# Kernel optimization log

Measured on AMD Instinct MI355X. Metric: run time of the kernel, lower is better.

Reference implementation:

```python
import jax, jax.numpy as jnp
import numpy as np

NUM_NODES = 100000
NUM_EDGES = 1600000
EMBED_DIM = 128
NUM_CLASSES = 2
NUM_LAYERS = 3


def setup_inputs() -> dict:
    key = jax.random.key(0)
    k_row, k_col, k_val, k_emb, k_a, k_w, k_b = jax.random.split(key, 7)
    node_indices = jnp.arange(NUM_NODES, dtype=jnp.int64 if jax.config.read('jax_enable_x64') else jnp.int32)
    adj_row = jax.random.randint(k_row, (NUM_EDGES,), 0, NUM_NODES)
    adj_col = jax.random.randint(k_col, (NUM_EDGES,), 0, NUM_NODES)
    # symmetric-normalized-ish positive edge weights
    adj_val = jax.random.uniform(k_val, (NUM_EDGES,), dtype=jnp.float32) * (1.0 / 16.0)
    embedding = jax.random.normal(k_emb, (NUM_NODES, EMBED_DIM), dtype=jnp.float32)
    alpha = jnp.ones((NUM_LAYERS + 1,), dtype=jnp.float32) / (NUM_LAYERS + 1)
    W = jax.random.normal(k_w, (EMBED_DIM, NUM_CLASSES), dtype=jnp.float32) * 0.05
    b = jnp.zeros((NUM_CLASSES,), dtype=jnp.float32)
    return {
        'node_indices': node_indices, 'adj_row': adj_row, 'adj_col': adj_col,
        'adj_val': adj_val, 'embedding': embedding, 'alpha': alpha, 'W': W, 'b': b,
    }


def reference(node_indices, adj_row, adj_col, adj_val, embedding, alpha, W, b):
    # x: [N, D] embedding lookup
    x = embedding[node_indices]
    a = jax.nn.softmax(alpha)
    # alpha-weighted running sum over propagation layers (dropout in eval mode = identity)
    acc = a[0] * x
    cur = x
    for i in range(NUM_LAYERS):
        # sparse SpMM: out[r] += val * cur[c] for each edge (r, c)
        msgs = adj_val[:, None] * cur[adj_col]          # [E, D]
        cur = jax.ops.segment_sum(msgs, adj_row, num_segments=NUM_NODES)
        acc = acc + a[i + 1] * cur
    return acc @ W + b  # [N, num_classes]
```

## Files before the change

kernel.cpp:

```cpp
#include <hip/hip_runtime.h>

#define GD(x,y) (((x)+(y)-1)/(y))

#define SH   7
#define BPR  (1 << SH)
#define G1   256
#define BS   256

__global__ void softmax_k(const float* __restrict__ alpha, float* __restrict__ a, int n){
    if (threadIdx.x == 0 && blockIdx.x == 0){
        float m = alpha[0];
        for (int i = 1; i < n; ++i) m = fmaxf(m, alpha[i]);
        float s = 0.f;
        for (int i = 0; i < n; ++i){ float e = expf(alpha[i] - m); a[i] = e; s += e; }
        float inv = 1.f / s;
        for (int i = 0; i < n; ++i) a[i] *= inv;
    }
}

__global__ void histb_k(const int* __restrict__ row, int* __restrict__ cnt,
                        int E, int NBK, int chunk){
    __shared__ int h[1024];
    for (int i = threadIdx.x; i < NBK; i += BS) h[i] = 0;
    __syncthreads();
    int s = blockIdx.x * chunk, e = min(E, s + chunk);
    for (int i = s + threadIdx.x; i < e; i += BS)
        atomicAdd(&h[row[i] >> SH], 1);
    __syncthreads();
    for (int i = threadIdx.x; i < NBK; i += BS)
        cnt[i * G1 + blockIdx.x] = h[i];
}

__global__ void scanA_k(const int* __restrict__ in, int* __restrict__ bsum, int M){
    __shared__ int lds[256];
    int t = threadIdx.x;
    int base = blockIdx.x * 1024 + t * 4;
    int s = 0;
    #pragma unroll
    for (int j = 0; j < 4; ++j) if (base + j < M) s += in[base + j];
    lds[t] = s; __syncthreads();
    for (int off = 128; off; off >>= 1){
        if (t < off) lds[t] += lds[t + off];
        __syncthreads();
    }
    if (t == 0) bsum[blockIdx.x] = lds[0];
}

__global__ void scanB_k(int* __restrict__ bsum, int NB){
    __shared__ int lds[1024];
    int t = threadIdx.x;
    int v = (t < NB) ? bsum[t] : 0;
    lds[t] = v; __syncthreads();
    for (int off = 1; off < 1024; off <<= 1){
        int add = (t >= off) ? lds[t - off] : 0;
        __syncthreads();
        lds[t] += add;
        __syncthreads();
    }
    if (t < NB) bsum[t] = lds[t] - v;
}

__global__ void scanC_k(const int* __restrict__ in, const int* __restrict__ bsum,
                        int* __restrict__ outx, int M){
    __shared__ int lds[256];
    int t = threadIdx.x;
    int base = blockIdx.x * 1024 + t * 4;
    int d[4]; int s = 0;
    #pragma unroll
    for (int j = 0; j < 4; ++j){ d[j] = (base + j < M) ? in[base + j] : 0; s += d[j]; }
    lds[t] = s; __syncthreads();
    for (int off = 1; off < 256; off <<= 1){
        int add = (t >= off) ? lds[t - off] : 0;
        __syncthreads();
        lds[t] += add;
        __syncthreads();
    }
    int run = bsum[blockIdx.x] + lds[t] - s;
    #pragma unroll
    for (int j = 0; j < 4; ++j){
        int i = base + j;
        if (i < M){ outx[i] = run; run += d[j]; }
    }
}

__global__ void bptr_k(const int* __restrict__ base, int* __restrict__ bptr, int NBK, int E){
    int b = blockIdx.x * blockDim.x + threadIdx.x;
    if (b < NBK) bptr[b] = base[b * G1];
    if (b == NBK) bptr[b] = E;
}

__global__ void fill3_k(const int* __restrict__ row, const int* __restrict__ col,
                        const float* __restrict__ val, const int* __restrict__ base,
                        int2* __restrict__ sep, int E, int NBK, int chunk){
    __shared__ int cur[1024];
    for (int i = threadIdx.x; i < NBK; i += BS)
        cur[i] = base[i * G1 + blockIdx.x];
    __syncthreads();
    int s = blockIdx.x * chunk, e = min(E, s + chunk);
    for (int i = s + threadIdx.x; i < e; i += BS){
        int r = row[i];
        int b = r >> SH;
        int pos = atomicAdd(&cur[b], 1);
        int2 pk;
        pk.x = col[i] | ((r & (BPR - 1)) << 17);
        pk.y = __float_as_int(val[i]);
        sep[pos] = pk;
    }
}

__global__ void proj_k(const float* __restrict__ emb, const int* __restrict__ idx,
                       const float* __restrict__ W, const float* __restrict__ b,
                       const float* __restrict__ a, float* __restrict__ y,
                       float* __restrict__ out, int N){
    int t = blockIdx.x * blockDim.x + threadIdx.x;
    int n = t >> 6;
    if (n >= N) return;
    int lane = t & 63;
    float2 x = ((const float2*)(emb + (size_t)idx[n] * 128))[lane];
    int d0 = 2 * lane;
    float s0 = x.x * W[d0 * 2]     + x.y * W[d0 * 2 + 2];
    float s1 = x.x * W[d0 * 2 + 1] + x.y * W[d0 * 2 + 3];
    for (int off = 32; off; off >>= 1){
        s0 += __shfl_down(s0, off);
        s1 += __shfl_down(s1, off);
    }
    if (lane == 0){
        float c = a[0];
        ((float2*)y)[n]   = make_float2(s0, s1);
        ((float2*)out)[n] = make_float2(b[0] + c * s0, b[1] + c * s1);
    }
}

__global__ void spmmb_k(const int* __restrict__ bptr, const int2* __restrict__ sep,
                        const float* __restrict__ y, float* __restrict__ nxt,
                        const float* __restrict__ a, int ai,
                        float* __restrict__ out, int N){
    __shared__ float acc[BPR * 2];
    int b = blockIdx.x;
    int t = threadIdx.x;
    acc[t] = 0.f;
    __syncthreads();
    int s = bptr[b], e = bptr[b + 1];
    for (int i = s + t; i < e; i += BS){
        int2 pk = sep[i];
        int c  = pk.x & 0x1FFFF;
        int rl = pk.x >> 17;
        float v = __int_as_float(pk.y);
        float2 m = ((const float2*)y)[c];
        atomicAdd(&acc[2 * rl],     v * m.x);
        atomicAdd(&acc[2 * rl + 1], v * m.y);
    }
    __syncthreads();
    int n = (b << SH) + (t >> 1);
    if (n < N){
        size_t gi = ((size_t)(b << SH)) * 2 + t;
        float z = acc[t];
        nxt[gi] = z;
        out[gi] += a[ai] * z;
    }
}

extern "C" void kernel_launch(void* const* d_in, const int* in_sizes, int n_in,
                              void* d_out, int out_size, void* d_ws, size_t ws_size,
                              hipStream_t stream) {
    const int*   node_idx = (const int*)  d_in[0];
    const int*   adj_row  = (const int*)  d_in[1];
    const int*   adj_col  = (const int*)  d_in[2];
    const float* adj_val  = (const float*)d_in[3];
    const float* emb      = (const float*)d_in[4];
    const float* alpha    = (const float*)d_in[5];
    const float* W        = (const float*)d_in[6];
    const float* b        = (const float*)d_in[7];
    float* out = (float*)d_out;

    const int N = in_sizes[0];
    const int E = in_sizes[1];
    const int L = in_sizes[5] - 1;
    const int NBK = GD(N, BPR);
    const int M = NBK * G1;
    const int NBA = GD(M, 1024);
    const int chunk = GD(E, G1);

    char* w = (char*)d_ws;
    float* y    = (float*)w;  w += (size_t)N * 2 * 4;
    float* nxt  = (float*)w;  w += (size_t)N * 2 * 4;
    int2*  sep  = (int2*)w;   w += (size_t)E * 8;
    int*   cnt  = (int*)w;    w += (size_t)M * 4;
    int*   bas  = (int*)w;    w += (size_t)M * 4;
    int*   bsum = (int*)w;    w += 4096;
    int*   bptr = (int*)w;    w += ((size_t)NBK + 2) * 4;
    float* a    = (float*)w;

    softmax_k<<<1, 64, 0, stream>>>(alpha, a, L + 1);

    histb_k<<<G1, BS, 0, stream>>>(adj_row, cnt, E, NBK, chunk);
    scanA_k<<<NBA, 256, 0, stream>>>(cnt, bsum, M);
    scanB_k<<<1, 1024, 0, stream>>>(bsum, NBA);
    scanC_k<<<NBA, 256, 0, stream>>>(cnt, bsum, bas, M);
    bptr_k<<<GD(NBK + 1, 256), 256, 0, stream>>>(bas, bptr, NBK, E);
    fill3_k<<<G1, BS, 0, stream>>>(adj_row, adj_col, adj_val, bas, sep, E, NBK, chunk);

    proj_k<<<GD(N * 64, 256), 256, 0, stream>>>(emb, node_idx, W, b, a, y, out, N);

    for (int i = 0; i < L; ++i){
        spmmb_k<<<NBK, BS, 0, stream>>>(bptr, sep, y, nxt, a, i + 1, out, N);
        float* tmp = y; y = nxt; nxt = tmp;
    }
}
```

Measured before the change: 141.7 us.

## Widen histogram grid, fold softmax into scan, drop bptr kernel, half-wave projection

Raises the histogram/fill grid from 256 to 1024 blocks so the binning passes have more parallelism, at the cost of a four times larger count matrix to scan. The separate softmax and bptr kernels are removed: softmax now runs on thread 0 of the single-block scan kernel, and the SpMM reads bucket bounds straight from the scanned base array. The projection kernel uses float4 loads with two nodes per wavefront, halving the thread count. SpMM splits the LDS accumulators into x/y arrays and writes float2 results.

```diff
diff --git a/kernel.cpp b/kernel.cpp
--- a/kernel.cpp
+++ b/kernel.cpp
@@ -4,19 +4,8 @@
 
 #define SH   7
 #define BPR  (1 << SH)
-#define G1   256
+#define G1   1024
 #define BS   256
-
-__global__ void softmax_k(const float* __restrict__ alpha, float* __restrict__ a, int n){
-    if (threadIdx.x == 0 && blockIdx.x == 0){
-        float m = alpha[0];
-        for (int i = 1; i < n; ++i) m = fmaxf(m, alpha[i]);
-        float s = 0.f;
-        for (int i = 0; i < n; ++i){ float e = expf(alpha[i] - m); a[i] = e; s += e; }
-        float inv = 1.f / s;
-        for (int i = 0; i < n; ++i) a[i] *= inv;
-    }
-}
 
 __global__ void histb_k(const int* __restrict__ row, int* __restrict__ cnt,
                         int E, int NBK, int chunk){
@@ -28,7 +17,7 @@
         atomicAdd(&h[row[i] >> SH], 1);
     __syncthreads();
     for (int i = threadIdx.x; i < NBK; i += BS)
-        cnt[i * G1 + blockIdx.x] = h[i];
+        cnt[(size_t)i * G1 + blockIdx.x] = h[i];
 }
 
 __global__ void scanA_k(const int* __restrict__ in, int* __restrict__ bsum, int M){
@@ -46,9 +35,18 @@
     if (t == 0) bsum[blockIdx.x] = lds[0];
 }
 
-__global__ void scanB_k(int* __restrict__ bsum, int NB){
+__global__ void scanB_k(int* __restrict__ bsum, int NB,
+                        const float* __restrict__ alpha, float* __restrict__ a, int na){
     __shared__ int lds[1024];
     int t = threadIdx.x;
+    if (t == 0){
+        float m = alpha[0];
+        for (int i = 1; i < na; ++i) m = fmaxf(m, alpha[i]);
+        float s = 0.f;
+        for (int i = 0; i < na; ++i){ float e = expf(alpha[i] - m); a[i] = e; s += e; }
+        float inv = 1.f / s;
+        for (int i = 0; i < na; ++i) a[i] *= inv;
+    }
     int v = (t < NB) ? bsum[t] : 0;
     lds[t] = v; __syncthreads();
     for (int off = 1; off < 1024; off <<= 1){
@@ -81,12 +79,6 @@
         int i = base + j;
         if (i < M){ outx[i] = run; run += d[j]; }
     }
-}
-
-__global__ void bptr_k(const int* __restrict__ base, int* __restrict__ bptr, int NBK, int E){
-    int b = blockIdx.x * blockDim.x + threadIdx.x;
-    if (b < NBK) bptr[b] = base[b * G1];
-    if (b == NBK) bptr[b] = E;
 }
 
 __global__ void fill3_k(const int* __restrict__ row, const int* __restrict__ col,
@@ -94,7 +86,7 @@
                         int2* __restrict__ sep, int E, int NBK, int chunk){
     __shared__ int cur[1024];
     for (int i = threadIdx.x; i < NBK; i += BS)
-        cur[i] = base[i * G1 + blockIdx.x];
+        cur[i] = base[(size_t)i * G1 + blockIdx.x];
     __syncthreads();
     int s = blockIdx.x * chunk, e = min(E, s + chunk);
     for (int i = s + threadIdx.x; i < e; i += BS){
@@ -113,50 +105,58 @@
                        const float* __restrict__ a, float* __restrict__ y,
                        float* __restrict__ out, int N){
     int t = blockIdx.x * blockDim.x + threadIdx.x;
-    int n = t >> 6;
+    int w = t >> 6;
+    int lane = t & 63;
+    int n = w * 2 + (lane >> 5);
     if (n >= N) return;
-    int lane = t & 63;
-    float2 x = ((const float2*)(emb + (size_t)idx[n] * 128))[lane];
-    int d0 = 2 * lane;
-    float s0 = x.x * W[d0 * 2]     + x.y * W[d0 * 2 + 2];
-    float s1 = x.x * W[d0 * 2 + 1] + x.y * W[d0 * 2 + 3];
-    for (int off = 32; off; off >>= 1){
-        s0 += __shfl_down(s0, off);
-        s1 += __shfl_down(s1, off);
-    }
-    if (lane == 0){
+    int sl = lane & 31;
+    float4 x = ((const float4*)(emb + (size_t)idx[n] * 128))[sl];
+    int d0 = 4 * sl;
+    float s0 = x.x * W[d0*2]   + x.y * W[d0*2+2] + x.z * W[d0*2+4] + x.w * W[d0*2+6];
+    float s1 = x.x * W[d0*2+1] + x.y * W[d0*2+3] + x.z * W[d0*2+5] + x.w * W[d0*2+7];
+    #pragma unroll
+    for (int off = 16; off; off >>= 1){
+        s0 += __shfl_down(s0, off, 32);
+        s1 += __shfl_down(s1, off, 32);
+    }
+    if (sl == 0){
         float c = a[0];
         ((float2*)y)[n]   = make_float2(s0, s1);
         ((float2*)out)[n] = make_float2(b[0] + c * s0, b[1] + c * s1);
     }
 }
 
-__global__ void spmmb_k(const int* __restrict__ bptr, const int2* __restrict__ sep,
+__global__ void spmmb_k(const int* __restrict__ bas, const int2* __restrict__ sep,
                         const float* __restrict__ y, float* __restrict__ nxt,
                         const float* __restrict__ a, int ai,
-                        float* __restrict__ out, int N){
-    __shared__ float acc[BPR * 2];
+                        float* __restrict__ out, int N, int NBK, int E){
+    __shared__ float accx[BPR];
+    __shared__ float accy[BPR];
     int b = blockIdx.x;
     int t = threadIdx.x;
-    acc[t] = 0.f;
-    __syncthreads();
-    int s = bptr[b], e = bptr[b + 1];
+    if (t < BPR){ accx[t] = 0.f; accy[t] = 0.f; }
+    __syncthreads();
+    int s = bas[(size_t)b * G1];
+    int e = (b + 1 < NBK) ? bas[(size_t)(b + 1) * G1] : E;
     for (int i = s + t; i < e; i += BS){
         int2 pk = sep[i];
         int c  = pk.x & 0x1FFFF;
         int rl = pk.x >> 17;
         float v = __int_as_float(pk.y);
         float2 m = ((const float2*)y)[c];
-        atomicAdd(&acc[2 * rl],     v * m.x);
-        atomicAdd(&acc[2 * rl + 1], v * m.y);
-    }
-    __syncthreads();
-    int n = (b << SH) + (t >> 1);
-    if (n < N){
-        size_t gi = ((size_t)(b << SH)) * 2 + t;
-        float z = acc[t];
-        nxt[gi] = z;
-        out[gi] += a[ai] * z;
+        atomicAdd(&accx[rl], v * m.x);
+        atomicAdd(&accy[rl], v * m.y);
+    }
+    __syncthreads();
+    if (t < BPR){
+        int n = (b << SH) + t;
+        if (n < N){
+            float2 z = make_float2(accx[t], accy[t]);
+            ((float2*)nxt)[n] = z;
+            float2 o = ((float2*)out)[n];
+            o.x += a[ai] * z.x; o.y += a[ai] * z.y;
+            ((float2*)out)[n] = o;
+        }
     }
 }
 
@@ -188,22 +188,18 @@
     int*   cnt  = (int*)w;    w += (size_t)M * 4;
     int*   bas  = (int*)w;    w += (size_t)M * 4;
     int*   bsum = (int*)w;    w += 4096;
-    int*   bptr = (int*)w;    w += ((size_t)NBK + 2) * 4;
     float* a    = (float*)w;
-
-    softmax_k<<<1, 64, 0, stream>>>(alpha, a, L + 1);
 
     histb_k<<<G1, BS, 0, stream>>>(adj_row, cnt, E, NBK, chunk);
     scanA_k<<<NBA, 256, 0, stream>>>(cnt, bsum, M);
-    scanB_k<<<1, 1024, 0, stream>>>(bsum, NBA);
+    scanB_k<<<1, 1024, 0, stream>>>(bsum, NBA, alpha, a, L + 1);
     scanC_k<<<NBA, 256, 0, stream>>>(cnt, bsum, bas, M);
-    bptr_k<<<GD(NBK + 1, 256), 256, 0, stream>>>(bas, bptr, NBK, E);
     fill3_k<<<G1, BS, 0, stream>>>(adj_row, adj_col, adj_val, bas, sep, E, NBK, chunk);
 
-    proj_k<<<GD(N * 64, 256), 256, 0, stream>>>(emb, node_idx, W, b, a, y, out, N);
+    proj_k<<<GD(N * 32, 256), 256, 0, stream>>>(emb, node_idx, W, b, a, y, out, N);
 
     for (int i = 0; i < L; ++i){
-        spmmb_k<<<NBK, BS, 0, stream>>>(bptr, sep, y, nxt, a, i + 1, out, N);
+        spmmb_k<<<NBK, BS, 0, stream>>>(bas, sep, y, nxt, a, i + 1, out, N, NBK, E);
         float* tmp = y; y = nxt; nxt = tmp;
     }
 }
```

Measured after the change: 136.7 us. -3.5%, faster.
